# Optimization experiments

Hardware: AMD Instinct MI355X
Metric: run time of the kernel (lower is better)

## Reference

```python
import jax, jax.numpy as jnp
import numpy as np

H = 16        # num_heads
K = 128       # head_k_dim
V = 128       # head_v_dim (expand_v = 1.0)
BT = 64       # chunk_size
BASE_LR = 0.1
EPS = 1e-05


def setup_inputs() -> dict:
    key = jax.random.key(0)
    ks = jax.random.split(key, 9)
    B, T, D = 2, 4096, 2048
    s = 0.02
    inputs = jax.random.normal(ks[0], (B, T, D), jnp.float32)
    Wq = jax.random.normal(ks[1], (H * K, D), jnp.float32) * s
    Wk = jax.random.normal(ks[2], (H * K, D), jnp.float32) * s
    Wv = jax.random.normal(ks[3], (H * V, D), jnp.float32) * s
    Weta = jax.random.normal(ks[4], (H, D), jnp.float32) * s
    Wtheta = jax.random.normal(ks[5], (H, D), jnp.float32) * s
    Wg = jax.random.normal(ks[6], (H * V, D), jnp.float32) * s
    norm_w = jnp.ones((V,), jnp.float32)
    Wo = jax.random.normal(ks[7], (D, H * V), jnp.float32) * s
    return {"inputs": inputs, "Wq": Wq, "Wk": Wk, "Wv": Wv, "Weta": Weta,
            "Wtheta": Wtheta, "Wg": Wg, "norm_w": norm_w, "Wo": Wo}


def _forward(inputs, Wq, Wk, Wv, Weta, Wtheta, Wg, norm_w, Wo):
    B, T, D = inputs.shape

    def proj_heads(W, d):
        # (B,T,D) @ (D,H*d) -> (B,H,T,d)
        return (inputs @ W.T).reshape(B, T, H, d).transpose(0, 2, 1, 3)

    q = proj_heads(Wq, K) * (K ** -0.5)
    k = proj_heads(Wk, K)
    v = proj_heads(Wv, V)

    eta = jax.nn.sigmoid(inputs @ Weta.T).transpose(0, 2, 1)          # (B,H,T)
    theta = BASE_LR * jax.nn.sigmoid(inputs @ Wtheta.T).transpose(0, 2, 1)

    NT = T // BT

    def chunkify(x, d):
        return x.reshape(B, H, NT, BT, d).transpose(2, 0, 1, 3, 4)    # (NT,B,H,BT,d)

    qs, kc_all, vs = chunkify(q, K), chunkify(k, K), chunkify(v, V)
    es = eta.reshape(B, H, NT, BT).transpose(2, 0, 1, 3)              # (NT,B,H,BT)
    ts = theta.reshape(B, H, NT, BT).transpose(2, 0, 1, 3)

    tril = jnp.tril(jnp.ones((BT, BT), bool))

    def step(W, xs):
        # W: (B,H,V,K) matrix-valued fast-weight state
        qc, kc, vc, ec, tc = xs
        e = jnp.einsum('bhtk,bhvk->bhtv', kc, W) - vc                  # prediction error
        lec = jnp.cumsum(jnp.log(jnp.clip(ec, 1e-8, None)), axis=-1)   # (B,H,BT) cum log-decay
        beta = jnp.where(tril,
                         jnp.exp(jnp.minimum(lec[..., :, None] - lec[..., None, :], 0.0)),
                         0.0)                                          # (B,H,BT,BT)
        qk = jnp.einsum('bhik,bhjk->bhij', qc, kc)
        theta_e = tc[..., None] * e                                    # (B,H,BT,V)
        z = (jnp.einsum('bhtk,bhvk->bhtv', qc * jnp.exp(lec)[..., None], W)
             - jnp.einsum('bhij,bhjv->bhiv', qk * beta, theta_e))
        e_decay = beta[:, :, -1, :, None] * theta_e                    # decay-to-chunk-end
        dw = jnp.einsum('bhtv,bhtk->bhvk', e_decay, kc)
        Wn = W * jnp.exp(lec[..., -1])[..., None, None] - dw
        return Wn, z

    W0 = jnp.zeros((B, H, V, K), inputs.dtype)
    W_fin, outs = jax.lax.scan(step, W0, (qs, kc_all, vs, es, ts))     # outs: (NT,B,H,BT,V)
    outs = outs.transpose(1, 2, 0, 3, 4).reshape(B, H, T, V).transpose(0, 2, 1, 3)  # (B,T,H,V)

    # gated RMS norm: rmsnorm(x) * weight * silu(g)
    g = (inputs @ Wg.T).reshape(B, T, H, V)
    rms = outs * jax.lax.rsqrt(jnp.mean(outs * outs, axis=-1, keepdims=True) + EPS)
    o = rms * norm_w * jax.nn.silu(g)
    return o.reshape(B, T, H * V) @ Wo.T                               # (B,T,D)


def reference(inputs, Wq, Wk, Wv, Weta, Wtheta, Wg, norm_w, Wo):
    return _forward(inputs, Wq, Wk, Wv, Weta, Wtheta, Wg, norm_w, Wo)
```

## Files before the change

kernel.cpp:

```cpp
#include <hip/hip_runtime.h>
#include <cstdint>
#include <cstddef>


typedef unsigned short u16b;
typedef __attribute__((ext_vector_type(8))) __bf16 bf16x8;
typedef __attribute__((ext_vector_type(4))) float  f32x4;

__device__ __forceinline__ float bf2f(u16b v){
  union { float f; uint32_t u; } x; x.u = ((uint32_t)v) << 16; return x.f;
}
__device__ __forceinline__ void split2(float f, u16b& h, u16b& l){
  uint32_t u = __float_as_uint(f);
  float hf = __uint_as_float(u & 0xFFFF0000u);
  h = (u16b)(u >> 16);
  l = (u16b)(__float_as_uint(f - hf) >> 16);
}
__device__ __forceinline__ f32x4 mfma16(bf16x8 a, bf16x8 b, f32x4 c){
  return __builtin_amdgcn_mfma_f32_16x16x32_bf16(a, b, c, 0, 0, 0);
}
__device__ __forceinline__ int ksw(int r, int c){
  return r*128 + (c ^ ((r & 7) << 3));
}

template<int AMODE, int OUTMODE>
__global__ __launch_bounds__(256) void gemm3(
    const float* __restrict__ Af,
    const u16b* __restrict__ Ah, const u16b* __restrict__ Al,
    const float* __restrict__ Bf,
    u16b* __restrict__ Ch, u16b* __restrict__ Cl, float* __restrict__ Cf,
    int M, int N, int Kd, float alpha)
{
  __shared__ u16b Ahs[128*32];
  __shared__ u16b Als[128*32];
  __shared__ u16b Bhs[128*32];
  __shared__ u16b Bls[128*32];
  const int m0 = blockIdx.y * 128;
  const int n0 = blockIdx.x * 128;
  const int tid  = threadIdx.x;
  const int wid  = tid >> 6;
  const int lane = tid & 63;
  const int wm = (wid & 1) * 64;
  const int wn = (wid >> 1) * 64;
  const int rw = lane & 15;
  const int kq = (lane >> 4) * 8;

  f32x4 acc[4][4] = {};

  for (int k0 = 0; k0 < Kd; k0 += 32){
    float4 fb[4];
#pragma unroll
    for (int it = 0; it < 4; it++){
      int idx = it*256 + tid;
      int rr = idx >> 3, c4 = (idx & 7) * 4;
      fb[it] = *(const float4*)(Bf + (size_t)(n0 + rr) * Kd + k0 + c4);
    }
    float4 fa[4];
    uint4  ua[4];
    if constexpr (AMODE == 0){
#pragma unroll
      for (int it = 0; it < 4; it++){
        int idx = it*256 + tid;
        int rr = idx >> 3, c4 = (idx & 7) * 4;
        fa[it] = *(const float4*)(Af + (size_t)(m0 + rr) * Kd + k0 + c4);
      }
    } else {
      int r0 = tid >> 2, c8 = (tid & 3) * 8;
      size_t offA = (size_t)(m0 + r0) * Kd + k0 + c8;
      ua[0] = *(const uint4*)(Ah + offA);
      ua[1] = *(const uint4*)(Ah + offA + (size_t)64*Kd);
      ua[2] = *(const uint4*)(Al + offA);
      ua[3] = *(const uint4*)(Al + offA + (size_t)64*Kd);
    }
    __syncthreads();
#pragma unroll
    for (int it = 0; it < 4; it++){
      int idx = it*256 + tid;
      int rr = idx >> 3, c4 = (idx & 7) * 4;
      float f[4] = {fb[it].x, fb[it].y, fb[it].z, fb[it].w};
      u16b h[4], l[4];
#pragma unroll
      for (int j = 0; j < 4; j++) split2(f[j], h[j], l[j]);
      *(uint2*)&Bhs[rr*32 + c4] = *(const uint2*)h;
      *(uint2*)&Bls[rr*32 + c4] = *(const uint2*)l;
    }
    if constexpr (AMODE == 0){
#pragma unroll
      for (int it = 0; it < 4; it++){
        int idx = it*256 + tid;
        int rr = idx >> 3, c4 = (idx & 7) * 4;
        float f[4] = {fa[it].x, fa[it].y, fa[it].z, fa[it].w};
        u16b h[4], l[4];
#pragma unroll
        for (int j = 0; j < 4; j++) split2(f[j], h[j], l[j]);
        *(uint2*)&Ahs[rr*32 + c4] = *(const uint2*)h;
        *(uint2*)&Als[rr*32 + c4] = *(const uint2*)l;
      }
    } else {
      int r0 = tid >> 2, c8 = (tid & 3) * 8;
      *(uint4*)&Ahs[r0*32 + c8]      = ua[0];
      *(uint4*)&Ahs[(64+r0)*32 + c8] = ua[1];
      *(uint4*)&Als[r0*32 + c8]      = ua[2];
      *(uint4*)&Als[(64+r0)*32 + c8] = ua[3];
    }
    __syncthreads();

    bf16x8 afh[4], afl[4], bfh[4], bfl[4];
#pragma unroll
    for (int i = 0; i < 4; i++){
      afh[i] = *(const bf16x8*)&Ahs[(wm + i*16 + rw)*32 + kq];
      afl[i] = *(const bf16x8*)&Als[(wm + i*16 + rw)*32 + kq];
    }
#pragma unroll
    for (int j = 0; j < 4; j++){
      bfh[j] = *(const bf16x8*)&Bhs[(wn + j*16 + rw)*32 + kq];
      bfl[j] = *(const bf16x8*)&Bls[(wn + j*16 + rw)*32 + kq];
    }
#pragma unroll
    for (int i = 0; i < 4; i++)
#pragma unroll
      for (int j = 0; j < 4; j++){
        f32x4 t = mfma16(afl[i], bfh[j], acc[i][j]);
        t = mfma16(afh[i], bfl[j], t);
        acc[i][j] = mfma16(afh[i], bfh[j], t);
      }
  }

  const int col  = lane & 15;
  const int quad = lane >> 4;
#pragma unroll
  for (int i = 0; i < 4; i++)
#pragma unroll
    for (int j = 0; j < 4; j++)
#pragma unroll
      for (int r = 0; r < 4; r++){
        int row = m0 + wm + i*16 + quad*4 + r;
        int c   = n0 + wn + j*16 + col;
        float v = acc[i][j][r] * alpha;
        if constexpr (OUTMODE == 0){
          u16b h, l; split2(v, h, l);
          Ch[(size_t)row * N + c] = h;
          Cl[(size_t)row * N + c] = l;
        } else {
          Cf[(size_t)row * N + c] = v;
        }
      }
}

__global__ __launch_bounds__(256) void etatheta_kernel(
    const float* __restrict__ x, const float* __restrict__ Weta,
    const float* __restrict__ Wtheta, float* __restrict__ eta, float* __restrict__ theta)
{
  __shared__ float xr[2048];
  const int bt = blockIdx.x;
  const int b = bt >> 12, t = bt & 4095;
  const float* xp = x + (size_t)bt * 2048;
  for (int i = threadIdx.x; i < 2048; i += 256) xr[i] = xp[i];
  __syncthreads();
  const int wid = threadIdx.x >> 6, lane = threadIdx.x & 63;
  for (int oi = 0; oi < 8; oi++){
    int og = wid*8 + oi;
    const float* wrow = (og < 16) ? (Weta + (size_t)og*2048)
                                  : (Wtheta + (size_t)(og-16)*2048);
    float acc = 0.f;
    for (int d = lane; d < 2048; d += 64) acc += xr[d] * wrow[d];
#pragma unroll
    for (int off = 32; off; off >>= 1) acc += __shfl_down(acc, off);
    if (lane == 0){
      float s = 1.f / (1.f + expf(-acc));
      if (og < 16) eta  [((size_t)(b*16 + og     ))*4096 + t] = s;
      else         theta[((size_t)(b*16 + og - 16))*4096 + t] = 0.1f * s;
    }
  }
}

__global__ __launch_bounds__(64) void decay_kernel(
    const float* __restrict__ eta, const float* __restrict__ th,
    float* __restrict__ lecb, float* __restrict__ eltb, float* __restrict__ wtb)
{
  const int bh = blockIdx.x, n = blockIdx.y, lane = threadIdx.x;
  size_t idx = (size_t)bh*4096 + n*64 + lane;
  float cum = logf(fmaxf(eta[idx], 1e-8f));
#pragma unroll
  for (int off = 1; off < 64; off <<= 1){
    float o = __shfl_up(cum, off);
    if (lane >= off) cum += o;
  }
  float lec63 = __shfl(cum, 63);
  lecb[idx] = cum;
  eltb[idx] = expf(cum);
  wtb[idx]  = expf(lec63 - cum) * th[idx];
}

#define WSTR 136
__global__ __launch_bounds__(512) void scan_kernel(
    const u16b* __restrict__ qh, const u16b* __restrict__ ql,
    const u16b* __restrict__ kh, const u16b* __restrict__ kl,
    const float* __restrict__ lecb, const float* __restrict__ eltb,
    const float* __restrict__ wtb,  const float* __restrict__ thb,
    float* vo)
{
  __shared__ u16b kh_s[64*128], kl_s[64*128];
  __shared__ u16b kTh_s[128*72], kTl_s[128*72];
  __shared__ u16b Wh[32*WSTR], Wl[32*WSTR];
  __shared__ u16b eh_s [32*72], el_s [32*72];
  __shared__ u16b ewh_s[32*72], ewl_s[32*72];
  __shared__ u16b Sh_s [64*72], Sl_s [64*72];
  __shared__ float v_s[64*36];
  __shared__ float dec_s[4*64];

  const int bh = blockIdx.x;
  const int b = bh >> 4, h = bh & 15;
  const int v0 = blockIdx.y * 32;
  const int tid  = threadIdx.x;
  const int wid  = tid >> 6;
  const int tw   = wid & 3;
  const int jh   = wid >> 2;
  const int lane = tid & 63;
  const int rw = lane & 15;
  const int kq = (lane >> 4) * 8;
  const int ccol  = lane & 15;
  const int cquad = lane >> 4;

  for (int i = tid; i < 32*WSTR; i += 512){ Wh[i] = 0; Wl[i] = 0; }

  const size_t rowbase = (size_t)b * 4096;
  const size_t decbase = (size_t)bh * 4096;
  const int sr0 = tid >> 4;
  const int sc8 = (tid & 15) * 8;
  const int rot = ((tid & 15) + ((lane >> 4) << 1)) & 7;

  for (int n = 0; n < 64; n++){
    const int tbase = n * 64;
    __syncthreads();

#pragma unroll
    for (int it = 0; it < 2; it++){
      int r = it*32 + sr0;
      size_t g = (rowbase + tbase + r) * 2048 + (size_t)h*128 + sc8;
      uint4 uh = *(const uint4*)&kh[g];
      uint4 ul = *(const uint4*)&kl[g];
      *(uint4*)&kh_s[ksw(r, sc8)] = uh;
      *(uint4*)&kl_s[ksw(r, sc8)] = ul;
      const u16b* ph = (const u16b*)&uh;
      const u16b* pl = (const u16b*)&ul;
#pragma unroll
      for (int s = 0; s < 8; s++){
        int i = (s + rot) & 7;
        kTh_s[(sc8 + i)*72 + r] = ph[i];
        kTl_s[(sc8 + i)*72 + r] = pl[i];
      }
    }
    {
      int r = tid >> 3, c4 = (tid & 7) * 4;
      size_t g = (rowbase + tbase + r) * 2048 + (size_t)h*128 + v0 + c4;
      *(float4*)&v_s[r*36 + c4] = *(const float4*)&vo[g];
    }
    if (tid < 256){
      const float* srcs[4] = {lecb, eltb, wtb, thb};
      dec_s[tid] = srcs[tid >> 6][decbase + tbase + (tid & 63)];
    }
    const size_t qg = (rowbase + tbase + tw*16 + rw) * 2048 + (size_t)h*128;
    bf16x8 qah[4], qal[4];
#pragma unroll
    for (int ks = 0; ks < 4; ks++){
      qah[ks] = *(const bf16x8*)(qh + qg + ks*32 + kq);
      qal[ks] = *(const bf16x8*)(ql + qg + ks*32 + kq);
    }
    __syncthreads();

    f32x4 eacc = {};
#pragma unroll
    for (int ks = 0; ks < 4; ks++){
      bf16x8 ah  = *(const bf16x8*)&kh_s[ksw(tw*16 + rw, ks*32 + kq)];
      bf16x8 al  = *(const bf16x8*)&kl_s[ksw(tw*16 + rw, ks*32 + kq)];
      bf16x8 bh_ = *(const bf16x8*)&Wh[(jh*16 + rw)*WSTR + ks*32 + kq];
      bf16x8 bl_ = *(const bf16x8*)&Wl[(jh*16 + rw)*WSTR + ks*32 + kq];
      f32x4 t = mfma16(al, bh_, eacc);
      t = mfma16(ah, bl_, t);
      eacc = mfma16(ah, bh_, t);
    }
    f32x4 qkacc[2] = {};
    f32x4 zqacc = {};
#pragma unroll
    for (int ks = 0; ks < 4; ks++){
#pragma unroll
      for (int j2 = 0; j2 < 2; j2++){
        int j4 = jh*2 + j2;
        bf16x8 bh_ = *(const bf16x8*)&kh_s[ksw(j4*16 + rw, ks*32 + kq)];
        bf16x8 bl_ = *(const bf16x8*)&kl_s[ksw(j4*16 + rw, ks*32 + kq)];
        f32x4 t = mfma16(qal[ks], bh_, qkacc[j2]);
        t = mfma16(qah[ks], bl_, t);
        qkacc[j2] = mfma16(qah[ks], bh_, t);
      }
      bf16x8 wh_ = *(const bf16x8*)&Wh[(jh*16 + rw)*WSTR + ks*32 + kq];
      bf16x8 wl_ = *(const bf16x8*)&Wl[(jh*16 + rw)*WSTR + ks*32 + kq];
      f32x4 t = mfma16(qal[ks], wh_, zqacc);
      t = mfma16(qah[ks], wl_, t);
      zqacc = mfma16(qah[ks], wh_, t);
    }
#pragma unroll
    for (int r = 0; r < 4; r++){
      int t  = tw*16 + cquad*4 + r;
      int vv = jh*16 + ccol;
      float e = eacc[r] - v_s[t*36 + vv];
      u16b h1, l1; split2(e, h1, l1);
      eh_s[vv*72 + t] = h1;  el_s[vv*72 + t] = l1;
      float ew = e * dec_s[128 + t];
      u16b h2, l2; split2(ew, h2, l2);
      ewh_s[vv*72 + t] = h2; ewl_s[vv*72 + t] = l2;
    }
#pragma unroll
    for (int j2 = 0; j2 < 2; j2++)
#pragma unroll
      for (int r = 0; r < 4; r++){
        int t  = tw*16 + cquad*4 + r;
        int jj = (jh*2 + j2)*16 + ccol;
        float s = 0.f;
        if (jj <= t)
          s = qkacc[j2][r] * __expf(fminf(dec_s[t] - dec_s[jj], 0.f)) * dec_s[192 + jj];
        u16b h1, l1; split2(s, h1, l1);
        Sh_s[t*72 + jj] = h1;  Sl_s[t*72 + jj] = l1;
      }
    __syncthreads();

    f32x4 seacc = {};
#pragma unroll
    for (int ks2 = 0; ks2 < 2; ks2++){
      bf16x8 ah  = *(const bf16x8*)&Sh_s[(tw*16 + rw)*72 + ks2*32 + kq];
      bf16x8 al  = *(const bf16x8*)&Sl_s[(tw*16 + rw)*72 + ks2*32 + kq];
      bf16x8 bh_ = *(const bf16x8*)&eh_s[(jh*16 + rw)*72 + ks2*32 + kq];
      bf16x8 bl_ = *(const bf16x8*)&el_s[(jh*16 + rw)*72 + ks2*32 + kq];
      f32x4 t = mfma16(al, bh_, seacc);
      t = mfma16(ah, bl_, t);
      seacc = mfma16(ah, bh_, t);
    }
#pragma unroll
    for (int r = 0; r < 4; r++){
      int t  = tw*16 + cquad*4 + r;
      int vv = jh*16 + ccol;
      float z = dec_s[64 + t]*zqacc[r] - seacc[r];
      vo[((rowbase + tbase + t)*16 + h)*128 + v0 + vv] = z;
    }
    f32x4 dwacc[2] = {};
    const int kcol = wid*16 + rw;
#pragma unroll
    for (int ks2 = 0; ks2 < 2; ks2++){
      bf16x8 bh_ = *(const bf16x8*)&kTh_s[kcol*72 + ks2*32 + kq];
      bf16x8 bl_ = *(const bf16x8*)&kTl_s[kcol*72 + ks2*32 + kq];
#pragma unroll
      for (int mi = 0; mi < 2; mi++){
        bf16x8 amh = *(const bf16x8*)&ewh_s[(mi*16 + rw)*72 + ks2*32 + kq];
        bf16x8 aml = *(const bf16x8*)&ewl_s[(mi*16 + rw)*72 + ks2*32 + kq];
        f32x4 t = mfma16(aml, bh_, dwacc[mi]);
        t = mfma16(amh, bl_, t);
        dwacc[mi] = mfma16(amh, bh_, t);
      }
    }
    float dfac = dec_s[64 + 63];
#pragma unroll
    for (int mi = 0; mi < 2; mi++)
#pragma unroll
      for (int r = 0; r < 4; r++){
        int vv = mi*16 + cquad*4 + r;
        int kk = wid*16 + ccol;
        int idx = vv*WSTR + kk;
        float w = bf2f(Wh[idx]) + bf2f(Wl[idx]);
        w = w*dfac - dwacc[mi][r];
        u16b h1, l1; split2(w, h1, l1);
        Wh[idx] = h1; Wl[idx] = l1;
      }
  }
}
#undef WSTR

__global__ __launch_bounds__(256) void norm_kernel(
    const float* __restrict__ outs, const float* __restrict__ g,
    const float* __restrict__ nw, u16b* __restrict__ ogh, u16b* __restrict__ ogl)
{
  const int bt = blockIdx.x;
  const int tid = threadIdx.x;
  size_t base = (size_t)bt*2048 + (size_t)tid*8;
  float4 x0 = *(const float4*)(outs + base);
  float4 x1 = *(const float4*)(outs + base + 4);
  float x[8] = {x0.x,x0.y,x0.z,x0.w,x1.x,x1.y,x1.z,x1.w};
  float ss = 0.f;
#pragma unroll
  for (int i = 0; i < 8; i++) ss += x[i]*x[i];
#pragma unroll
  for (int off = 1; off < 16; off <<= 1) ss += __shfl_xor(ss, off);
  float rs = rsqrtf(ss*(1.f/128.f) + 1e-5f);
  float4 g0 = *(const float4*)(g + base);
  float4 g1 = *(const float4*)(g + base + 4);
  float gg[8] = {g0.x,g0.y,g0.z,g0.w,g1.x,g1.y,g1.z,g1.w};
  int nwb = (tid & 15)*8;
  u16b oh[8], ol[8];
#pragma unroll
  for (int i = 0; i < 8; i++){
    float sig = 1.f / (1.f + __expf(-gg[i]));
    float v = x[i]*rs*nw[nwb+i]*gg[i]*sig;
    split2(v, oh[i], ol[i]);
  }
  *(uint4*)(ogh + base) = *(const uint4*)oh;
  *(uint4*)(ogl + base) = *(const uint4*)ol;
}

extern "C" void kernel_launch(void* const* d_in, const int* in_sizes, int n_in,
                              void* d_out, int out_size, void* d_ws, size_t ws_size,
                              hipStream_t stream)
{
  (void)in_sizes; (void)n_in; (void)out_size; (void)ws_size;
  const float* x    = (const float*)d_in[0];
  const float* Wq   = (const float*)d_in[1];
  const float* Wk   = (const float*)d_in[2];
  const float* Wv   = (const float*)d_in[3];
  const float* Weta = (const float*)d_in[4];
  const float* Wth  = (const float*)d_in[5];
  const float* Wg   = (const float*)d_in[6];
  const float* nw   = (const float*)d_in[7];
  const float* Wo   = (const float*)d_in[8];
  float* out = (float*)d_out;

  const size_t SZ = (size_t)8192*2048;
  const size_t DS = (size_t)2*16*4096;
  u16b* ws = (u16b*)d_ws;
  u16b* qhb = ws;            u16b* qlb = qhb + SZ;
  u16b* khb = qlb + SZ;      u16b* klb = khb + SZ;
  float* vob  = (float*)(klb + SZ);
  float* etab = vob + SZ;
  float* thb  = etab + DS;
  float* lecb = thb  + DS;
  float* eltb = lecb + DS;
  float* wtb  = eltb + DS;
  float* gfb  = (float*)khb;
  u16b* ogh = qhb; u16b* ogl = qlb;

  dim3 gg(16, 64);
  etatheta_kernel<<<8192, 256, 0, stream>>>(x, Weta, Wth, etab, thb);
  decay_kernel<<<dim3(32,64), 64, 0, stream>>>(etab, thb, lecb, eltb, wtb);
  gemm3<0,0><<<gg, 256, 0, stream>>>(x, nullptr, nullptr, Wq, qhb, qlb, nullptr,
                                     8192, 2048, 2048, 0.08838834764831843f);
  gemm3<0,0><<<gg, 256, 0, stream>>>(x, nullptr, nullptr, Wk, khb, klb, nullptr,
                                     8192, 2048, 2048, 1.f);
  gemm3<0,1><<<gg, 256, 0, stream>>>(x, nullptr, nullptr, Wv, nullptr, nullptr, vob,
                                     8192, 2048, 2048, 1.f);
  scan_kernel<<<dim3(32,4), 512, 0, stream>>>(qhb, qlb, khb, klb,
                                              lecb, eltb, wtb, thb, vob);
  gemm3<0,1><<<gg, 256, 0, stream>>>(x, nullptr, nullptr, Wg, nullptr, nullptr, gfb,
                                     8192, 2048, 2048, 1.f);
  norm_kernel<<<8192, 256, 0, stream>>>(vob, gfb, nw, ogh, ogl);
  gemm3<1,1><<<gg, 256, 0, stream>>>(nullptr, ogh, ogl, Wo, nullptr, nullptr, out,
                                     8192, 2048, 2048, 1.f);
}
```

Baseline: 2.011 ms.

## Pre-split GEMM operands to bf16 hi/lo and load them directly into LDS

Adds a split kernel that converts x and the weight matrices into bf16 high/low halves once, instead of re-splitting fp32 tiles inside every GEMM k-iteration. The new GEMM loads those halves straight into LDS with global_load_lds and reads them back through an XOR-swizzled layout. It also remaps the block index for L2-friendly rasterization and stages the output tile through LDS so global stores are wide and coalesced. The cost is extra split passes and workspace aliasing (x halves stored in the output buffer, weight halves in scratch regions), which depends on careful ordering of the kernels.

```diff
diff --git a/kernel.cpp b/kernel.cpp
--- a/kernel.cpp
+++ b/kernel.cpp
@@ -4,6 +4,7 @@
 
 
 typedef unsigned short u16b;
+typedef uint32_t u32;
 typedef __attribute__((ext_vector_type(8))) __bf16 bf16x8;
 typedef __attribute__((ext_vector_type(4))) float  f32x4;
 
@@ -19,24 +20,53 @@
 __device__ __forceinline__ f32x4 mfma16(bf16x8 a, bf16x8 b, f32x4 c){
   return __builtin_amdgcn_mfma_f32_16x16x32_bf16(a, b, c, 0, 0, 0);
 }
+__device__ __forceinline__ void gl16(const void* g, void* l){
+  __builtin_amdgcn_global_load_lds(
+      (const __attribute__((address_space(1))) u32*)g,
+      (__attribute__((address_space(3))) u32*)l, 16, 0, 0);
+}
 __device__ __forceinline__ int ksw(int r, int c){
   return r*128 + (c ^ ((r & 7) << 3));
 }
 
-template<int AMODE, int OUTMODE>
-__global__ __launch_bounds__(256) void gemm3(
-    const float* __restrict__ Af,
+__global__ __launch_bounds__(256) void split_kernel(
+    const float* __restrict__ src, u16b* __restrict__ dh, u16b* __restrict__ dl,
+    int n8)
+{
+  int i = blockIdx.x*256 + threadIdx.x;
+  if (i >= n8) return;
+  const float4* s4 = (const float4*)src;
+  float4 a = s4[2*(size_t)i], b = s4[2*(size_t)i + 1];
+  float f[8] = {a.x,a.y,a.z,a.w,b.x,b.y,b.z,b.w};
+  u16b h[8], l[8];
+#pragma unroll
+  for (int j = 0; j < 8; j++) split2(f[j], h[j], l[j]);
+  *(uint4*)(dh + (size_t)i*8) = *(const uint4*)h;
+  *(uint4*)(dl + (size_t)i*8) = *(const uint4*)l;
+}
+
+template<int BMODE, int OUTMODE>
+__global__ __launch_bounds__(256) void gemm3v(
     const u16b* __restrict__ Ah, const u16b* __restrict__ Al,
+    const u16b* __restrict__ Bh, const u16b* __restrict__ Bl,
     const float* __restrict__ Bf,
     u16b* __restrict__ Ch, u16b* __restrict__ Cl, float* __restrict__ Cf,
     int M, int N, int Kd, float alpha)
 {
-  __shared__ u16b Ahs[128*32];
-  __shared__ u16b Als[128*32];
-  __shared__ u16b Bhs[128*32];
-  __shared__ u16b Bls[128*32];
-  const int m0 = blockIdx.y * 128;
-  const int n0 = blockIdx.x * 128;
+  (void)M;
+  __shared__ __align__(16) u16b smem[16384];
+  u16b* Ahs = smem;
+  u16b* Als = smem + 4096;
+  u16b* Bhs = smem + 8192;
+  u16b* Bls = smem + 12288;
+
+  const int cpx = gridDim.x >> 3;
+  const int flat = blockIdx.x;
+  const int swz = (flat & 7) * cpx + (flat >> 3);
+  const int nb = N >> 7;
+  const int m0 = (swz / nb) * 128;
+  const int n0 = (swz % nb) * 128;
+
   const int tid  = threadIdx.x;
   const int wid  = tid >> 6;
   const int lane = tid & 63;
@@ -44,77 +74,71 @@
   const int wn = (wid >> 1) * 64;
   const int rw = lane & 15;
   const int kq = (lane >> 4) * 8;
+  const int sx = ((rw >> 1) & 3) << 3;
+
+  const int srow = tid >> 2;
+  const int scol = ((tid & 3) * 8) ^ (((tid >> 3) & 3) << 3);
+  const u16b* gA0 = Ah + (size_t)(m0 + srow)*Kd + scol;
+  const u16b* gA1 = gA0 + (size_t)64*Kd;
+  const u16b* gAl0 = Al + (size_t)(m0 + srow)*Kd + scol;
+  const u16b* gAl1 = gAl0 + (size_t)64*Kd;
+  const u16b* gB0 = nullptr; const u16b* gB1 = nullptr;
+  const u16b* gBl0 = nullptr; const u16b* gBl1 = nullptr;
+  if constexpr (BMODE == 1){
+    gB0  = Bh + (size_t)(n0 + srow)*Kd + scol;
+    gB1  = gB0 + (size_t)64*Kd;
+    gBl0 = Bl + (size_t)(n0 + srow)*Kd + scol;
+    gBl1 = gBl0 + (size_t)64*Kd;
+  }
 
   f32x4 acc[4][4] = {};
 
   for (int k0 = 0; k0 < Kd; k0 += 32){
     float4 fb[4];
-#pragma unroll
-    for (int it = 0; it < 4; it++){
-      int idx = it*256 + tid;
-      int rr = idx >> 3, c4 = (idx & 7) * 4;
-      fb[it] = *(const float4*)(Bf + (size_t)(n0 + rr) * Kd + k0 + c4);
-    }
-    float4 fa[4];
-    uint4  ua[4];
-    if constexpr (AMODE == 0){
+    if constexpr (BMODE == 0){
 #pragma unroll
       for (int it = 0; it < 4; it++){
         int idx = it*256 + tid;
         int rr = idx >> 3, c4 = (idx & 7) * 4;
-        fa[it] = *(const float4*)(Af + (size_t)(m0 + rr) * Kd + k0 + c4);
-      }
+        fb[it] = *(const float4*)(Bf + (size_t)(n0 + rr) * Kd + k0 + c4);
+      }
+    }
+    __syncthreads();
+    gl16(gA0  + k0, Ahs + tid*8);
+    gl16(gA1  + k0, Ahs + 2048 + tid*8);
+    gl16(gAl0 + k0, Als + tid*8);
+    gl16(gAl1 + k0, Als + 2048 + tid*8);
+    if constexpr (BMODE == 1){
+      gl16(gB0  + k0, Bhs + tid*8);
+      gl16(gB1  + k0, Bhs + 2048 + tid*8);
+      gl16(gBl0 + k0, Bls + tid*8);
+      gl16(gBl1 + k0, Bls + 2048 + tid*8);
     } else {
-      int r0 = tid >> 2, c8 = (tid & 3) * 8;
-      size_t offA = (size_t)(m0 + r0) * Kd + k0 + c8;
-      ua[0] = *(const uint4*)(Ah + offA);
-      ua[1] = *(const uint4*)(Ah + offA + (size_t)64*Kd);
-      ua[2] = *(const uint4*)(Al + offA);
-      ua[3] = *(const uint4*)(Al + offA + (size_t)64*Kd);
-    }
-    __syncthreads();
-#pragma unroll
-    for (int it = 0; it < 4; it++){
-      int idx = it*256 + tid;
-      int rr = idx >> 3, c4 = (idx & 7) * 4;
-      float f[4] = {fb[it].x, fb[it].y, fb[it].z, fb[it].w};
-      u16b h[4], l[4];
-#pragma unroll
-      for (int j = 0; j < 4; j++) split2(f[j], h[j], l[j]);
-      *(uint2*)&Bhs[rr*32 + c4] = *(const uint2*)h;
-      *(uint2*)&Bls[rr*32 + c4] = *(const uint2*)l;
-    }
-    if constexpr (AMODE == 0){
 #pragma unroll
       for (int it = 0; it < 4; it++){
         int idx = it*256 + tid;
         int rr = idx >> 3, c4 = (idx & 7) * 4;
-        float f[4] = {fa[it].x, fa[it].y, fa[it].z, fa[it].w};
+        int cs = c4 ^ (((rr >> 1) & 3) << 3);
+        float f[4] = {fb[it].x, fb[it].y, fb[it].z, fb[it].w};
         u16b h[4], l[4];
 #pragma unroll
         for (int j = 0; j < 4; j++) split2(f[j], h[j], l[j]);
-        *(uint2*)&Ahs[rr*32 + c4] = *(const uint2*)h;
-        *(uint2*)&Als[rr*32 + c4] = *(const uint2*)l;
-      }
-    } else {
-      int r0 = tid >> 2, c8 = (tid & 3) * 8;
-      *(uint4*)&Ahs[r0*32 + c8]      = ua[0];
-      *(uint4*)&Ahs[(64+r0)*32 + c8] = ua[1];
-      *(uint4*)&Als[r0*32 + c8]      = ua[2];
-      *(uint4*)&Als[(64+r0)*32 + c8] = ua[3];
+        *(uint2*)&Bhs[rr*32 + cs] = *(const uint2*)h;
+        *(uint2*)&Bls[rr*32 + cs] = *(const uint2*)l;
+      }
     }
     __syncthreads();
 
     bf16x8 afh[4], afl[4], bfh[4], bfl[4];
 #pragma unroll
     for (int i = 0; i < 4; i++){
-      afh[i] = *(const bf16x8*)&Ahs[(wm + i*16 + rw)*32 + kq];
-      afl[i] = *(const bf16x8*)&Als[(wm + i*16 + rw)*32 + kq];
+      afh[i] = *(const bf16x8*)&Ahs[(wm + i*16 + rw)*32 + (kq ^ sx)];
+      afl[i] = *(const bf16x8*)&Als[(wm + i*16 + rw)*32 + (kq ^ sx)];
     }
 #pragma unroll
     for (int j = 0; j < 4; j++){
-      bfh[j] = *(const bf16x8*)&Bhs[(wn + j*16 + rw)*32 + kq];
-      bfl[j] = *(const bf16x8*)&Bls[(wn + j*16 + rw)*32 + kq];
+      bfh[j] = *(const bf16x8*)&Bhs[(wn + j*16 + rw)*32 + (kq ^ sx)];
+      bfl[j] = *(const bf16x8*)&Bls[(wn + j*16 + rw)*32 + (kq ^ sx)];
     }
 #pragma unroll
     for (int i = 0; i < 4; i++)
@@ -126,25 +150,46 @@
       }
   }
 
-  const int col  = lane & 15;
-  const int quad = lane >> 4;
-#pragma unroll
-  for (int i = 0; i < 4; i++)
+  float* Bnc = (float*)smem;
+  const int ccol  = lane & 15;
+  const int cquad = lane >> 4;
+  const int brb = ((wid & 1) << 4) + cquad*4;
+  const int br2 = tid >> 3, c0 = (tid & 7) * 16;
+#pragma unroll
+  for (int i = 0; i < 4; i++){
+    __syncthreads();
 #pragma unroll
     for (int j = 0; j < 4; j++)
 #pragma unroll
-      for (int r = 0; r < 4; r++){
-        int row = m0 + wm + i*16 + quad*4 + r;
-        int c   = n0 + wn + j*16 + col;
-        float v = acc[i][j][r] * alpha;
-        if constexpr (OUTMODE == 0){
-          u16b h, l; split2(v, h, l);
-          Ch[(size_t)row * N + c] = h;
-          Cl[(size_t)row * N + c] = l;
-        } else {
-          Cf[(size_t)row * N + c] = v;
-        }
-      }
+      for (int r = 0; r < 4; r++)
+        Bnc[(brb + r)*132 + wn + j*16 + ccol] = acc[i][j][r];
+    __syncthreads();
+    const int rowg = m0 + ((br2 >> 4) << 6) + i*16 + (br2 & 15);
+    float4 x0 = *(const float4*)&Bnc[br2*132 + c0];
+    float4 x1 = *(const float4*)&Bnc[br2*132 + c0 + 4];
+    float4 x2 = *(const float4*)&Bnc[br2*132 + c0 + 8];
+    float4 x3 = *(const float4*)&Bnc[br2*132 + c0 + 12];
+    float v[16] = {x0.x,x0.y,x0.z,x0.w, x1.x,x1.y,x1.z,x1.w,
+                   x2.x,x2.y,x2.z,x2.w, x3.x,x3.y,x3.z,x3.w};
+#pragma unroll
+    for (int e = 0; e < 16; e++) v[e] *= alpha;
+    if constexpr (OUTMODE == 0){
+      u16b h[16], l[16];
+#pragma unroll
+      for (int e = 0; e < 16; e++) split2(v[e], h[e], l[e]);
+      size_t off = (size_t)rowg * N + n0 + c0;
+      *(uint4*)(Ch + off)     = *(const uint4*)&h[0];
+      *(uint4*)(Ch + off + 8) = *(const uint4*)&h[8];
+      *(uint4*)(Cl + off)     = *(const uint4*)&l[0];
+      *(uint4*)(Cl + off + 8) = *(const uint4*)&l[8];
+    } else {
+      size_t off = (size_t)rowg * N + n0 + c0;
+      *(float4*)(Cf + off)      = *(const float4*)&v[0];
+      *(float4*)(Cf + off + 4)  = *(const float4*)&v[4];
+      *(float4*)(Cf + off + 8)  = *(const float4*)&v[8];
+      *(float4*)(Cf + off + 12) = *(const float4*)&v[12];
+    }
+  }
 }
 
 __global__ __launch_bounds__(256) void etatheta_kernel(
@@ -422,6 +467,7 @@
   float* out = (float*)d_out;
 
   const size_t SZ = (size_t)8192*2048;
+  const size_t WZ = (size_t)2048*2048;
   const size_t DS = (size_t)2*16*4096;
   u16b* ws = (u16b*)d_ws;
   u16b* qhb = ws;            u16b* qlb = qhb + SZ;
@@ -435,20 +481,37 @@
   float* gfb  = (float*)khb;
   u16b* ogh = qhb; u16b* ogl = qlb;
 
-  dim3 gg(16, 64);
+  u16b* xh = (u16b*)d_out;   u16b* xl = xh + SZ;
+  u16b* wsQh = khb;        u16b* wsQl = khb + WZ;
+  u16b* wsKh = (u16b*)vob; u16b* wsKl = wsKh + WZ;
+  u16b* wsGh = qhb;        u16b* wsGl = qhb + WZ;
+  u16b* wsOh = khb;        u16b* wsOl = khb + WZ;
+
+  dim3 gg(1024);
+  split_kernel<<<8192, 256, 0, stream>>>(x, xh, xl, (int)(SZ/8));
   etatheta_kernel<<<8192, 256, 0, stream>>>(x, Weta, Wth, etab, thb);
   decay_kernel<<<dim3(32,64), 64, 0, stream>>>(etab, thb, lecb, eltb, wtb);
-  gemm3<0,0><<<gg, 256, 0, stream>>>(x, nullptr, nullptr, Wq, qhb, qlb, nullptr,
-                                     8192, 2048, 2048, 0.08838834764831843f);
-  gemm3<0,0><<<gg, 256, 0, stream>>>(x, nullptr, nullptr, Wk, khb, klb, nullptr,
-                                     8192, 2048, 2048, 1.f);
-  gemm3<0,1><<<gg, 256, 0, stream>>>(x, nullptr, nullptr, Wv, nullptr, nullptr, vob,
-                                     8192, 2048, 2048, 1.f);
+
+  split_kernel<<<2048, 256, 0, stream>>>(Wq, wsQh, wsQl, (int)(WZ/8));
+  gemm3v<1,0><<<gg, 256, 0, stream>>>(xh, xl, wsQh, wsQl, nullptr,
+                                      qhb, qlb, nullptr,
+                                      8192, 2048, 2048, 0.08838834764831843f);
+  split_kernel<<<2048, 256, 0, stream>>>(Wk, wsKh, wsKl, (int)(WZ/8));
+  gemm3v<1,0><<<gg, 256, 0, stream>>>(xh, xl, wsKh, wsKl, nullptr,
+                                      khb, klb, nullptr,
+                                      8192, 2048, 2048, 1.f);
+  gemm3v<0,1><<<gg, 256, 0, stream>>>(xh, xl, nullptr, nullptr, Wv,
+                                      nullptr, nullptr, vob,
+                                      8192, 2048, 2048, 1.f);
   scan_kernel<<<dim3(32,4), 512, 0, stream>>>(qhb, qlb, khb, klb,
                                               lecb, eltb, wtb, thb, vob);
-  gemm3<0,1><<<gg, 256, 0, stream>>>(x, nullptr, nullptr, Wg, nullptr, nullptr, gfb,
-                                     8192, 2048, 2048, 1.f);
+  split_kernel<<<2048, 256, 0, stream>>>(Wg, wsGh, wsGl, (int)(WZ/8));
+  gemm3v<1,1><<<gg, 256, 0, stream>>>(xh, xl, wsGh, wsGl, nullptr,
+                                      nullptr, nullptr, gfb,
+                                      8192, 2048, 2048, 1.f);
   norm_kernel<<<8192, 256, 0, stream>>>(vob, gfb, nw, ogh, ogl);
-  gemm3<1,1><<<gg, 256, 0, stream>>>(nullptr, ogh, ogl, Wo, nullptr, nullptr, out,
-                                     8192, 2048, 2048, 1.f);
-}
+  split_kernel<<<2048, 256, 0, stream>>>(Wo, wsOh, wsOl, (int)(WZ/8));
+  gemm3v<1,1><<<gg, 256, 0, stream>>>(ogh, ogl, wsOh, wsOl, nullptr,
+                                      nullptr, nullptr, out,
+                                      8192, 2048, 2048, 1.f);
+}
```

Result: faster. 1.842 ms (-8.4%).
